# Kernel optimization log

Measured on AMD Instinct MI355X. Metric: run time of the kernel, lower is better.

The kernel has to match this reference:

```python
import jax, jax.numpy as jnp
import numpy as np

N_NODES = 100000

def gcn_conv(x, edge_index, W, b, n_nodes):
    # GCNConv: add self-loops, symmetric normalization D^-1/2 A D^-1/2, then linear.
    loops = jnp.arange(n_nodes, dtype=edge_index.dtype)
    row = jnp.concatenate([edge_index[0], loops])  # source nodes
    col = jnp.concatenate([edge_index[1], loops])  # destination nodes
    deg = jax.ops.segment_sum(jnp.ones_like(col, dtype=x.dtype), col, num_segments=n_nodes)
    dinv = jnp.where(deg > 0, jax.lax.rsqrt(deg), 0.0)
    norm = dinv[row] * dinv[col]                   # [E']
    h = x @ W                                      # [N, out] project first (out dim small)
    msgs = h[row] * norm[:, None]                  # gather + scale
    out = jax.ops.segment_sum(msgs, col, num_segments=n_nodes)  # scatter-add
    return out + b

def setup_inputs() -> dict:
    key = jax.random.key(0)
    k1, k2, k3, k4, k5, k6 = jax.random.split(key, 6)
    in_dim, hid, out_dim = 512, 16, 16
    x = jax.random.normal(k1, (N_NODES, in_dim), dtype=jnp.float32)
    edge_index = jax.random.randint(k2, (2, 3200000), 0, N_NODES, dtype=jnp.int64)
    # Glorot-style init for weights, zero bias (GCNConv defaults)
    W1 = jax.random.normal(k3, (in_dim, hid), dtype=jnp.float32) * (1.0 / np.sqrt(in_dim))
    b1 = jnp.zeros((hid,), dtype=jnp.float32)
    W2 = jax.random.normal(k4, (hid, out_dim), dtype=jnp.float32) * (1.0 / np.sqrt(hid))
    b2 = jnp.zeros((out_dim,), dtype=jnp.float32)
    return {"x": x, "edge_index": edge_index, "W1": W1, "b1": b1, "W2": W2, "b2": b2}

def reference(x, edge_index, W1, b1, W2, b2):
    h = jax.nn.relu(gcn_conv(x, edge_index, W1, b1, N_NODES))
    # dropout is identity in eval mode
    logits = gcn_conv(h, edge_index, W2, b2, N_NODES)
    return jax.nn.log_softmax(logits, axis=1)
```

## Files before the change

kernel.cpp:

```cpp
#include <hip/hip_runtime.h>
#include <cstddef>

typedef unsigned int uint32;
typedef short bf16x8 __attribute__((ext_vector_type(8)));
typedef float f32x4 __attribute__((ext_vector_type(4)));

#define BCAP 5120
#define NBLK 256

__device__ __forceinline__ unsigned short f2bf(float f) {
  unsigned u = __float_as_uint(f);
  unsigned r = (u + 0x7FFFu + ((u >> 16) & 1u)) >> 16;
  return (unsigned short)r;
}
__device__ __forceinline__ float bf_lo(uint32 u) { return __uint_as_float(u << 16); }
__device__ __forceinline__ float bf_hi(uint32 u) { return __uint_as_float(u & 0xFFFF0000u); }

__global__ __launch_bounds__(256) void k_init(
    int* __restrict__ bcur, int NB, const float* __restrict__ W1,
    unsigned short* __restrict__ wfrag) {
  int zb = (NB + 255) >> 8;
  int b = blockIdx.x;
  if (b < zb) {
    int i = b * 256 + threadIdx.x;
    if (i < NB) bcur[i] = i * BCAP;
  } else {
    int i = (b - zb) * 256 + threadIdx.x;
    if (i < 8192) {
      int j = i & 7, o = (i >> 3) & 15, g = (i >> 7) & 3, kt = i >> 9;
      wfrag[i] = f2bf(W1[(kt * 32 + g * 8 + j) * 16 + o]);
    }
  }
}

__global__ __launch_bounds__(1024) void k_bfill(
    const int* __restrict__ row, const int* __restrict__ col,
    int* __restrict__ bcur, int* __restrict__ bedges, int E, int NB, int chunk) {
  __shared__ int s[1024];
  for (int j = threadIdx.x; j < NB; j += 1024) s[j] = 0;
  __syncthreads();
  int lo = blockIdx.x * chunk;
  int hi = lo + chunk; if (hi > E) hi = E;
  for (int k = lo + threadIdx.x; k < hi; k += 1024) atomicAdd(&s[col[k] >> 7], 1);
  __syncthreads();
  for (int j = threadIdx.x; j < NB; j += 1024) {
    int h = s[j];
    s[j] = h ? atomicAdd(&bcur[j], h) : 0;
  }
  __syncthreads();
  for (int k = lo + threadIdx.x; k < hi; k += 1024) {
    int c = col[k];
    int b = c >> 7;
    int slot = atomicAdd(&s[b], 1);
    if (slot < (b + 1) * BCAP)
      bedges[slot] = ((c & 127) << 17) | row[k];
  }
}

__global__ __launch_bounds__(128) void k_bdeg(
    const int* __restrict__ bcur, const int* __restrict__ bedges,
    float* __restrict__ dinv, int n) {
  __shared__ int c[128];
  int b = blockIdx.x, t = threadIdx.x;
  c[t] = 0;
  __syncthreads();
  int k0 = b * BCAP;
  int k1 = bcur[b]; if (k1 > k0 + BCAP) k1 = k0 + BCAP;
  for (int k = k0 + t; k < k1; k += 128)
    atomicAdd(&c[((unsigned)bedges[k]) >> 17], 1);
  __syncthreads();
  int node = b * 128 + t;
  if (node < n) dinv[node] = rsqrtf(1.0f + (float)c[t]);
}

#define GCAP 2048
#define CAPL 48
template <int MODE>
__global__ __launch_bounds__(256) void k_gagg(
    const int* __restrict__ bcur, const int* __restrict__ bedges,
    const uint4* __restrict__ mb,
    float* __restrict__ agg, unsigned short* __restrict__ msgs_out,
    const float* __restrict__ dinv, const float* __restrict__ b1,
    const float* __restrict__ W2, const float* __restrict__ b2, int n) {
  __shared__ int lsrt[CAPL * 128];
  __shared__ int curs[128];
  __shared__ int ovf[128];
  __shared__ int novf;
  __shared__ float w2s[256];
  __shared__ float b1s[16];
  int b = blockIdx.x, t = threadIdx.x;
  if (MODE == 1) {
    w2s[t] = W2[t];
    if (t < 16) b1s[t] = b1[t];
  }
  int j = t >> 1, h = t & 1;
  int node = b * 128 + j;
  float a0 = 0.f, a1 = 0.f, a2 = 0.f, a3 = 0.f;
  float a4 = 0.f, a5 = 0.f, a6 = 0.f, a7 = 0.f;
  if (node < n) {
    float4 sA = *(const float4*)(agg + (size_t)node * 16 + h * 8);
    float4 sB = *(const float4*)(agg + (size_t)node * 16 + h * 8 + 4);
    a0 = sA.x; a1 = sA.y; a2 = sA.z; a3 = sA.w;
    a4 = sB.x; a5 = sB.y; a6 = sB.z; a7 = sB.w;
  }
  int k0 = b * BCAP;
  int k1 = bcur[b]; if (k1 > k0 + BCAP) k1 = k0 + BCAP;
  const uint4* mbh = mb + h;
  for (int base = k0; base < k1; base += GCAP) {
    int cnt = k1 - base; if (cnt > GCAP) cnt = GCAP;
    if (t < 128) curs[t] = 0;
    if (t == 0) novf = 0;
    __syncthreads();
    for (int idx = t; idx < cnt; idx += 256) {
      unsigned e = (unsigned)bedges[base + idx];
      int lc = e >> 17;
      int slot = atomicAdd(&curs[lc], 1);
      if (slot < CAPL) lsrt[slot * 128 + lc] = (int)(e & 0x1FFFF);
      else {
        int oi = atomicAdd(&novf, 1);
        if (oi < 128) ovf[oi] = (int)e;
      }
    }
    __syncthreads();
    int len = curs[j]; if (len > CAPL) len = CAPL;
    int k = 0;
    for (; k + 4 <= len; k += 4) {
      int r0 = lsrt[(k + 0) * 128 + j], r1 = lsrt[(k + 1) * 128 + j];
      int r2 = lsrt[(k + 2) * 128 + j], r3 = lsrt[(k + 3) * 128 + j];
      uint4 v0 = mbh[(size_t)r0 * 2];
      uint4 v1 = mbh[(size_t)r1 * 2];
      uint4 v2 = mbh[(size_t)r2 * 2];
      uint4 v3 = mbh[(size_t)r3 * 2];
      a0 += (bf_lo(v0.x) + bf_lo(v1.x)) + (bf_lo(v2.x) + bf_lo(v3.x));
      a1 += (bf_hi(v0.x) + bf_hi(v1.x)) + (bf_hi(v2.x) + bf_hi(v3.x));
      a2 += (bf_lo(v0.y) + bf_lo(v1.y)) + (bf_lo(v2.y) + bf_lo(v3.y));
      a3 += (bf_hi(v0.y) + bf_hi(v1.y)) + (bf_hi(v2.y) + bf_hi(v3.y));
      a4 += (bf_lo(v0.z) + bf_lo(v1.z)) + (bf_lo(v2.z) + bf_lo(v3.z));
      a5 += (bf_hi(v0.z) + bf_hi(v1.z)) + (bf_hi(v2.z) + bf_hi(v3.z));
      a6 += (bf_lo(v0.w) + bf_lo(v1.w)) + (bf_lo(v2.w) + bf_lo(v3.w));
      a7 += (bf_hi(v0.w) + bf_hi(v1.w)) + (bf_hi(v2.w) + bf_hi(v3.w));
    }
    for (; k < len; ++k) {
      uint4 v = mbh[(size_t)lsrt[k * 128 + j] * 2];
      a0 += bf_lo(v.x); a1 += bf_hi(v.x);
      a2 += bf_lo(v.y); a3 += bf_hi(v.y);
      a4 += bf_lo(v.z); a5 += bf_hi(v.z);
      a6 += bf_lo(v.w); a7 += bf_hi(v.w);
    }
    int no = novf; if (no > 128) no = 128;
    for (int i = 0; i < no; ++i) {
      unsigned e = (unsigned)ovf[i];
      if ((int)(e >> 17) == j) {
        uint4 v = mbh[(size_t)(e & 0x1FFFF) * 2];
        a0 += bf_lo(v.x); a1 += bf_hi(v.x);
        a2 += bf_lo(v.y); a3 += bf_hi(v.y);
        a4 += bf_lo(v.z); a5 += bf_hi(v.z);
        a6 += bf_lo(v.w); a7 += bf_hi(v.w);
      }
    }
    __syncthreads();
  }
  if (node < n) {
    float tot[8] = {a0, a1, a2, a3, a4, a5, a6, a7};
    float di = dinv[node];
    if (MODE == 1) {
      float hh[8];
#pragma unroll
      for (int f = 0; f < 8; ++f)
        hh[f] = fmaxf(fmaf(di, tot[f], b1s[h * 8 + f]), 0.0f);
      float gp[16];
#pragma unroll
      for (int o = 0; o < 16; ++o) gp[o] = 0.0f;
#pragma unroll
      for (int f = 0; f < 8; ++f) {
        float hf = hh[f];
        const float* wrow = &w2s[(h * 8 + f) * 16];
#pragma unroll
        for (int o = 0; o < 16; ++o) gp[o] = fmaf(hf, wrow[o], gp[o]);
      }
      float gv[8];
#pragma unroll
      for (int f = 0; f < 8; ++f) {
        float keep = h ? gp[8 + f] : gp[f];
        float send = h ? gp[f] : gp[8 + f];
        gv[f] = (keep + __shfl_xor(send, 1, 64)) * di;
      }
      uint32 u0 = (uint32)f2bf(gv[0]) | ((uint32)f2bf(gv[1]) << 16);
      uint32 u1 = (uint32)f2bf(gv[2]) | ((uint32)f2bf(gv[3]) << 16);
      uint32 u2 = (uint32)f2bf(gv[4]) | ((uint32)f2bf(gv[5]) << 16);
      uint32 u3 = (uint32)f2bf(gv[6]) | ((uint32)f2bf(gv[7]) << 16);
      uint4 pk; pk.x = u0; pk.y = u1; pk.z = u2; pk.w = u3;
      ((uint4*)msgs_out)[(size_t)node * 2 + h] = pk;
      float4* aw = (float4*)(agg + (size_t)node * 16 + h * 8);
      aw[0] = make_float4(gv[0], gv[1], gv[2], gv[3]);
      aw[1] = make_float4(gv[4], gv[5], gv[6], gv[7]);
    } else {
      float v[8];
#pragma unroll
      for (int f = 0; f < 8; ++f) v[f] = fmaf(di, tot[f], b2[h * 8 + f]);
      float m8 = v[0];
#pragma unroll
      for (int f = 1; f < 8; ++f) m8 = fmaxf(m8, v[f]);
      float m = fmaxf(m8, __shfl_xor(m8, 1, 64));
      float s8 = 0.0f;
#pragma unroll
      for (int f = 0; f < 8; ++f) s8 += expf(v[f] - m);
      float s = s8 + __shfl_xor(s8, 1, 64);
      float ls = logf(s) + m;
      float4* aw = (float4*)(agg + (size_t)node * 16 + h * 8);
      aw[0] = make_float4(v[0] - ls, v[1] - ls, v[2] - ls, v[3] - ls);
      aw[1] = make_float4(v[4] - ls, v[5] - ls, v[6] - ls, v[7] - ls);
    }
  }
}

__global__ __launch_bounds__(256) void k_gemm1_mfma(
    const float* __restrict__ x, const uint4* __restrict__ wf4,
    const float* __restrict__ dinv, unsigned short* __restrict__ msgsb,
    float* __restrict__ agg, int n) {
  int wave = threadIdx.x >> 6, lane = threadIdx.x & 63;
  int m = lane & 15, g = lane >> 4;
  int r0 = (blockIdx.x * 4 + wave) * 16;
  if (r0 >= n) return;

  union BU { uint4 u; bf16x8 v; };
  BU bfr[16];
#pragma unroll
  for (int kt = 0; kt < 16; ++kt) bfr[kt].u = wf4[kt * 64 + g * 16 + m];

  int row = r0 + m;
  int lrow = (row < n) ? row : (n - 1);
  const float* xr = x + (size_t)lrow * 512 + g * 8;

  f32x4 acc = {0.f, 0.f, 0.f, 0.f};
#pragma unroll
  for (int kt = 0; kt < 16; ++kt) {
    float4 xa = *(const float4*)(xr + kt * 32);
    float4 xb = *(const float4*)(xr + kt * 32 + 4);
    union { uint32 u[4]; bf16x8 v; } a;
    a.u[0] = (uint32)f2bf(xa.x) | ((uint32)f2bf(xa.y) << 16);
    a.u[1] = (uint32)f2bf(xa.z) | ((uint32)f2bf(xa.w) << 16);
    a.u[2] = (uint32)f2bf(xb.x) | ((uint32)f2bf(xb.y) << 16);
    a.u[3] = (uint32)f2bf(xb.z) | ((uint32)f2bf(xb.w) << 16);
    acc = __builtin_amdgcn_mfma_f32_16x16x32_bf16(a.v, bfr[kt].v, acc, 0, 0, 0);
  }

#pragma unroll
  for (int j = 0; j < 4; ++j) {
    int orow = r0 + g * 4 + j;
    if (orow < n) {
      float v = acc[j] * dinv[orow];
      agg[(size_t)orow * 16 + m] = v;
      msgsb[(size_t)orow * 16 + m] = f2bf(v);
    }
  }
}


__global__ void k_deg_init(float* __restrict__ deg, int n) {
  int i = blockIdx.x * 256 + threadIdx.x;
  if (i < n) deg[i] = 1.0f;
}

__global__ void k_deg_count(const int* __restrict__ col, float* __restrict__ deg, int E) {
  int e = blockIdx.x * 256 + threadIdx.x;
  if (e < E) atomicAdd(&deg[col[e]], 1.0f);
}

__global__ void k_rsqrt_inplace(float* __restrict__ deg, int n) {
  int i = blockIdx.x * 256 + threadIdx.x;
  if (i < n) deg[i] = rsqrtf(deg[i]);
}

__global__ void k_scatter(const int* __restrict__ row, const int* __restrict__ col,
                          const float* __restrict__ src, float* __restrict__ agg, int E) {
  int t = blockIdx.x * 256 + threadIdx.x;
  int e = t >> 2, q = t & 3;
  if (e >= E) return;
  int r = row[e];
  int c = col[e];
  float4 v = ((const float4*)(src + (size_t)r * 16))[q];
  float* dst = agg + (size_t)c * 16 + q * 4;
  atomicAdd(dst + 0, v.x);
  atomicAdd(dst + 1, v.y);
  atomicAdd(dst + 2, v.z);
  atomicAdd(dst + 3, v.w);
}

__global__ void k_transposeW1(const float* __restrict__ W1, float* __restrict__ wt) {
  int i = blockIdx.x * 256 + threadIdx.x;
  if (i < 512 * 16) {
    int e = i >> 4, f = i & 15;
    wt[f * 512 + e] = W1[i];
  }
}

__global__ __launch_bounds__(256) void k_gemm1(
    const float* __restrict__ x, const float* __restrict__ wt_g,
    const float* __restrict__ dinv,
    float* __restrict__ msgsf, float* __restrict__ agg, int n) {
  __shared__ float4 wt4[16 * 128];
  const float4* wg4 = (const float4*)wt_g;
  for (int k = threadIdx.x; k < 2048; k += 256) wt4[k] = wg4[k];
  __syncthreads();

  int wave = threadIdx.x >> 6, lane = threadIdx.x & 63;
  int r0 = blockIdx.x * 8 + wave * 2;
  if (r0 >= n) return;
  int r1 = (r0 + 1 < n) ? (r0 + 1) : r0;

  const float4* x0 = (const float4*)(x + (size_t)r0 * 512);
  const float4* x1 = (const float4*)(x + (size_t)r1 * 512);
  float4 xa0 = x0[lane], xb0 = x0[64 + lane];
  float4 xa1 = x1[lane], xb1 = x1[64 + lane];

  float acc0[16], acc1[16];
#pragma unroll
  for (int f = 0; f < 16; ++f) {
    float4 wa = wt4[f * 128 + lane];
    float4 wb = wt4[f * 128 + 64 + lane];
    acc0[f] = xa0.x * wa.x + xa0.y * wa.y + xa0.z * wa.z + xa0.w * wa.w +
              xb0.x * wb.x + xb0.y * wb.y + xb0.z * wb.z + xb0.w * wb.w;
    acc1[f] = xa1.x * wa.x + xa1.y * wa.y + xa1.z * wa.z + xa1.w * wa.w +
              xb1.x * wb.x + xb1.y * wb.y + xb1.z * wb.z + xb1.w * wb.w;
  }

#pragma unroll
  for (int s = 0; s < 4; ++s) {
    const int mask = 1 << s;
    const int hm = 8 >> s;
    bool up = (lane & mask) != 0;
#pragma unroll
    for (int i = 0; i < hm; ++i) {
      float s0 = up ? acc0[i] : acc0[i + hm];
      float s1 = up ? acc1[i] : acc1[i + hm];
      float g0 = __shfl_xor(s0, mask, 64);
      float g1 = __shfl_xor(s1, mask, 64);
      acc0[i] = (up ? acc0[i + hm] : acc0[i]) + g0;
      acc1[i] = (up ? acc1[i + hm] : acc1[i]) + g1;
    }
  }
  acc0[0] += __shfl_xor(acc0[0], 16, 64);
  acc0[0] += __shfl_xor(acc0[0], 32, 64);
  acc1[0] += __shfl_xor(acc1[0], 16, 64);
  acc1[0] += __shfl_xor(acc1[0], 32, 64);

  int grp = lane >> 4;
  if (grp < 2) {
    int row = r0 + grp;
    if (row < n) {
      int l4 = lane & 15;
      int f = ((l4 & 1) << 3) | ((l4 & 2) << 1) | ((l4 & 4) >> 1) | ((l4 & 8) >> 3);
      float v = (grp == 0 ? acc0[0] : acc1[0]) * dinv[row];
      msgsf[(size_t)row * 16 + f] = v;
      agg[(size_t)row * 16 + f] = v;
    }
  }
}

__global__ __launch_bounds__(256) void k_mid(
    float* __restrict__ agg, const float* __restrict__ dinv,
    const float* __restrict__ b1, const float* __restrict__ W2,
    float* __restrict__ gpf, int n) {
  __shared__ float w2s[256];
  __shared__ float b1s[16];
  if (threadIdx.x < 256) w2s[threadIdx.x] = W2[threadIdx.x];
  if (threadIdx.x < 16) b1s[threadIdx.x] = b1[threadIdx.x];
  __syncthreads();
  int i = blockIdx.x * 256 + threadIdx.x;
  if (i >= n) return;
  float di = dinv[i];
  float h[16];
  const float4* a4 = (const float4*)(agg + (size_t)i * 16);
#pragma unroll
  for (int q = 0; q < 4; ++q) {
    float4 v = a4[q];
    h[q * 4 + 0] = v.x; h[q * 4 + 1] = v.y; h[q * 4 + 2] = v.z; h[q * 4 + 3] = v.w;
  }
#pragma unroll
  for (int f = 0; f < 16; ++f) h[f] = fmaxf(fmaf(di, h[f], b1s[f]), 0.0f);
  float g[16];
#pragma unroll
  for (int o = 0; o < 16; ++o) g[o] = 0.0f;
#pragma unroll
  for (int f = 0; f < 16; ++f) {
    float hf = h[f];
#pragma unroll
    for (int o = 0; o < 16; ++o) g[o] = fmaf(hf, w2s[f * 16 + o], g[o]);
  }
  float4* gA = (float4*)(gpf + (size_t)i * 16);
  float4* gB = (float4*)(agg + (size_t)i * 16);
#pragma unroll
  for (int q = 0; q < 4; ++q) {
    float4 v;
    v.x = g[q * 4 + 0] * di; v.y = g[q * 4 + 1] * di;
    v.z = g[q * 4 + 2] * di; v.w = g[q * 4 + 3] * di;
    gA[q] = v;
    gB[q] = v;
  }
}

__global__ __launch_bounds__(256) void k_final(
    float* __restrict__ agg, const float* __restrict__ dinv,
    const float* __restrict__ b2, int n) {
  int i = blockIdx.x * 256 + threadIdx.x;
  if (i >= n) return;
  float di = dinv[i];
  float v[16];
  const float4* a4 = (const float4*)(agg + (size_t)i * 16);
#pragma unroll
  for (int q = 0; q < 4; ++q) {
    float4 t = a4[q];
    v[q * 4 + 0] = t.x; v[q * 4 + 1] = t.y; v[q * 4 + 2] = t.z; v[q * 4 + 3] = t.w;
  }
#pragma unroll
  for (int f = 0; f < 16; ++f) v[f] = fmaf(di, v[f], b2[f]);
  float m = v[0];
#pragma unroll
  for (int f = 1; f < 16; ++f) m = fmaxf(m, v[f]);
  float s = 0.0f;
#pragma unroll
  for (int f = 0; f < 16; ++f) s += expf(v[f] - m);
  float ls = logf(s) + m;
  float4* o4 = (float4*)(agg + (size_t)i * 16);
#pragma unroll
  for (int q = 0; q < 4; ++q) {
    float4 t;
    t.x = v[q * 4 + 0] - ls; t.y = v[q * 4 + 1] - ls;
    t.z = v[q * 4 + 2] - ls; t.w = v[q * 4 + 3] - ls;
    o4[q] = t;
  }
}

extern "C" void kernel_launch(void* const* d_in, const int* in_sizes, int n_in,
                              void* d_out, int out_size, void* d_ws, size_t ws_size,
                              hipStream_t stream) {
  const float* x = (const float*)d_in[0];
  const int* ei = (const int*)d_in[1];
  const float* W1 = (const float*)d_in[2];
  const float* b1 = (const float*)d_in[3];
  const float* W2 = (const float*)d_in[4];
  const float* b2 = (const float*)d_in[5];
  float* out = (float*)d_out;

  int n = in_sizes[0] / 512;
  int E = in_sizes[1] / 2;
  const int* row = ei;
  const int* col = ei + E;
  int NB = (n + 127) >> 7;

  auto align1k = [](size_t v) { return (v + 1023) & ~(size_t)1023; };
  char* ws = (char*)d_ws;
  size_t o = 0;
  float* dinv  = (float*)(ws + o); o += align1k((size_t)n * 4);
  unsigned short* wfrag = (unsigned short*)(ws + o); o += align1k(8192 * 2);
  int* bcur    = (int*)(ws + o);   o += align1k((size_t)NB * 4);
  int* bedges  = (int*)(ws + o);   o += align1k((size_t)NB * BCAP * 4);
  unsigned short* msgsb1 = (unsigned short*)(ws + o); o += align1k((size_t)n * 16 * 2);
  unsigned short* msgsb2 = (unsigned short*)(ws + o); o += align1k((size_t)n * 16 * 2);
  size_t needed = o;

  float* agg = out;
  int nb_n = (n + 255) / 256;
  int nb_e = (E + 255) / 256;
  int nb_e4 = (E * 4 + 255) / 256;

  if (ws_size >= needed && n <= 131072 && NB <= 1024) {
    int chunk = (E + NBLK - 1) / NBLK;
    int zb = (NB + 255) >> 8;
    k_init<<<zb + 32, 256, 0, stream>>>(bcur, NB, W1, wfrag);
    k_bfill<<<NBLK, 1024, 0, stream>>>(row, col, bcur, bedges, E, NB, chunk);
    k_bdeg<<<NB, 128, 0, stream>>>(bcur, bedges, dinv, n);
    k_gemm1_mfma<<<(n + 63) / 64, 256, 0, stream>>>(
        x, (const uint4*)wfrag, dinv, msgsb1, agg, n);
    k_gagg<1><<<NB, 256, 0, stream>>>(
        bcur, bedges, (const uint4*)msgsb1, agg, msgsb2, dinv, b1, W2, b2, n);
    k_gagg<2><<<NB, 256, 0, stream>>>(
        bcur, bedges, (const uint4*)msgsb2, agg, nullptr, dinv, b1, W2, b2, n);
  } else {
    size_t o2 = 0;
    float* dinv2 = (float*)(ws + o2); o2 += align1k((size_t)n * 4);
    float* wtg2  = (float*)(ws + o2); o2 += 32768;
    float* msgs2 = (float*)(ws + o2);
    k_deg_init<<<nb_n, 256, 0, stream>>>(dinv2, n);
    k_deg_count<<<nb_e, 256, 0, stream>>>(col, dinv2, E);
    k_rsqrt_inplace<<<nb_n, 256, 0, stream>>>(dinv2, n);
    k_transposeW1<<<32, 256, 0, stream>>>(W1, wtg2);
    k_gemm1<<<(n + 7) / 8, 256, 0, stream>>>(x, wtg2, dinv2, msgs2, agg, n);
    k_scatter<<<nb_e4, 256, 0, stream>>>(row, col, msgs2, agg, E);
    k_mid<<<nb_n, 256, 0, stream>>>(agg, dinv2, b1, W2, msgs2, n);
    k_scatter<<<nb_e4, 256, 0, stream>>>(row, col, msgs2, agg, E);
    k_final<<<nb_n, 256, 0, stream>>>(agg, dinv2, b2, n);
  }
}
```

Baseline: 154.6 us.

## Fuse degree, both aggregations into one cooperative kernel with grid syncs

Replaces the degree kernel and two aggregation kernels with one cooperative kernel. It builds each block's local edge lists in shared memory once, computes dinv, and uses grid syncs between the layer-1 and layer-2 aggregation phases. Because the GEMM now runs before dinv exists, the source-side dinv scaling is applied during aggregation through an extra dinv gather per edge. This saves launches and the repeated edge bucketing, but adds grid-wide barriers, per-edge dinv loads and a larger shared-memory list, which may lower occupancy. NB (~782 blocks) must all be co-resident, otherwise the code falls back to the old kernels.

```diff
diff --git a/kernel.cpp b/kernel.cpp
--- a/kernel.cpp
+++ b/kernel.cpp
@@ -1,5 +1,8 @@
 #include <hip/hip_runtime.h>
+#include <hip/hip_cooperative_groups.h>
 #include <cstddef>
+
+namespace cg = cooperative_groups;
 
 typedef unsigned int uint32;
 typedef short bf16x8 __attribute__((ext_vector_type(8)));
@@ -7,6 +10,7 @@
 
 #define BCAP 5120
 #define NBLK 256
+#define CAPL 72
 
 __device__ __forceinline__ unsigned short f2bf(float f) {
   unsigned u = __float_as_uint(f);
@@ -57,72 +61,182 @@
   }
 }
 
-__global__ __launch_bounds__(128) void k_bdeg(
+__global__ __launch_bounds__(256) void k_gemm1_mfma(
+    const float* __restrict__ x, const uint4* __restrict__ wf4,
+    unsigned short* __restrict__ msgsb, float* __restrict__ agg, int n) {
+  int wave = threadIdx.x >> 6, lane = threadIdx.x & 63;
+  int m = lane & 15, g = lane >> 4;
+  int r0 = (blockIdx.x * 4 + wave) * 16;
+  if (r0 >= n) return;
+
+  union BU { uint4 u; bf16x8 v; };
+  BU bfr[16];
+#pragma unroll
+  for (int kt = 0; kt < 16; ++kt) bfr[kt].u = wf4[kt * 64 + g * 16 + m];
+
+  int row = r0 + m;
+  int lrow = (row < n) ? row : (n - 1);
+  const float* xr = x + (size_t)lrow * 512 + g * 8;
+
+  f32x4 acc = {0.f, 0.f, 0.f, 0.f};
+#pragma unroll
+  for (int kt = 0; kt < 16; ++kt) {
+    float4 xa = *(const float4*)(xr + kt * 32);
+    float4 xb = *(const float4*)(xr + kt * 32 + 4);
+    union { uint32 u[4]; bf16x8 v; } a;
+    a.u[0] = (uint32)f2bf(xa.x) | ((uint32)f2bf(xa.y) << 16);
+    a.u[1] = (uint32)f2bf(xa.z) | ((uint32)f2bf(xa.w) << 16);
+    a.u[2] = (uint32)f2bf(xb.x) | ((uint32)f2bf(xb.y) << 16);
+    a.u[3] = (uint32)f2bf(xb.z) | ((uint32)f2bf(xb.w) << 16);
+    acc = __builtin_amdgcn_mfma_f32_16x16x32_bf16(a.v, bfr[kt].v, acc, 0, 0, 0);
+  }
+#pragma unroll
+  for (int j = 0; j < 4; ++j) {
+    int orow = r0 + g * 4 + j;
+    if (orow < n) {
+      agg[(size_t)orow * 16 + m] = acc[j];
+      msgsb[(size_t)orow * 16 + m] = f2bf(acc[j]);
+    }
+  }
+}
+
+__global__ __launch_bounds__(256) void k_coop(
     const int* __restrict__ bcur, const int* __restrict__ bedges,
-    float* __restrict__ dinv, int n) {
-  __shared__ int c[128];
-  int b = blockIdx.x, t = threadIdx.x;
-  c[t] = 0;
-  __syncthreads();
-  int k0 = b * BCAP;
-  int k1 = bcur[b]; if (k1 > k0 + BCAP) k1 = k0 + BCAP;
-  for (int k = k0 + t; k < k1; k += 128)
-    atomicAdd(&c[((unsigned)bedges[k]) >> 17], 1);
-  __syncthreads();
-  int node = b * 128 + t;
-  if (node < n) dinv[node] = rsqrtf(1.0f + (float)c[t]);
-}
-
-#define GCAP 2048
-#define CAPL 48
-template <int MODE>
-__global__ __launch_bounds__(256) void k_gagg(
-    const int* __restrict__ bcur, const int* __restrict__ bedges,
-    const uint4* __restrict__ mb,
-    float* __restrict__ agg, unsigned short* __restrict__ msgs_out,
-    const float* __restrict__ dinv, const float* __restrict__ b1,
-    const float* __restrict__ W2, const float* __restrict__ b2, int n) {
+    const uint4* __restrict__ mb1, unsigned short* __restrict__ msgsb2,
+    float* __restrict__ agg, float* __restrict__ dinv,
+    const float* __restrict__ b1, const float* __restrict__ W2,
+    const float* __restrict__ b2, int n) {
   __shared__ int lsrt[CAPL * 128];
   __shared__ int curs[128];
   __shared__ int ovf[128];
   __shared__ int novf;
   __shared__ float w2s[256];
   __shared__ float b1s[16];
+  cg::grid_group grid = cg::this_grid();
   int b = blockIdx.x, t = threadIdx.x;
-  if (MODE == 1) {
-    w2s[t] = W2[t];
-    if (t < 16) b1s[t] = b1[t];
-  }
+  w2s[t] = W2[t];
+  if (t < 16) b1s[t] = b1[t];
+  if (t < 128) curs[t] = 0;
+  if (t == 0) novf = 0;
+  __syncthreads();
+
+  int k0 = b * BCAP;
+  int cnt = bcur[b] - k0; if (cnt > BCAP) cnt = BCAP; if (cnt < 0) cnt = 0;
+  for (int idx = t; idx < cnt; idx += 256) {
+    unsigned e = (unsigned)bedges[k0 + idx];
+    int lc = e >> 17;
+    int slot = atomicAdd(&curs[lc], 1);
+    if (slot < CAPL) lsrt[slot * 128 + lc] = (int)(e & 0x1FFFF);
+    else {
+      int oi = atomicAdd(&novf, 1);
+      if (oi < 128) ovf[oi] = (int)e;
+    }
+  }
+  __syncthreads();
+  if (t < 128) {
+    int node = b * 128 + t;
+    if (node < n) dinv[node] = rsqrtf(1.0f + (float)curs[t]);
+  }
+  grid.sync();
+
   int j = t >> 1, h = t & 1;
   int node = b * 128 + j;
-  float a0 = 0.f, a1 = 0.f, a2 = 0.f, a3 = 0.f;
-  float a4 = 0.f, a5 = 0.f, a6 = 0.f, a7 = 0.f;
+  float di = (node < n) ? dinv[node] : 0.0f;
+  int len = 0;
+  if (node < n) { len = curs[j]; if (len > CAPL) len = CAPL; }
+  int no = novf; if (no > 128) no = 128;
+
+  {
+    float a0 = 0.f, a1 = 0.f, a2 = 0.f, a3 = 0.f;
+    float a4 = 0.f, a5 = 0.f, a6 = 0.f, a7 = 0.f;
+    if (node < n) {
+      float4 sA = *(const float4*)(agg + (size_t)node * 16 + h * 8);
+      float4 sB = *(const float4*)(agg + (size_t)node * 16 + h * 8 + 4);
+      a0 = di * sA.x; a1 = di * sA.y; a2 = di * sA.z; a3 = di * sA.w;
+      a4 = di * sB.x; a5 = di * sB.y; a6 = di * sB.z; a7 = di * sB.w;
+      const uint4* mbh = mb1 + h;
+      int k = 0;
+      for (; k + 4 <= len; k += 4) {
+        int r0 = lsrt[(k + 0) * 128 + j], r1 = lsrt[(k + 1) * 128 + j];
+        int r2 = lsrt[(k + 2) * 128 + j], r3 = lsrt[(k + 3) * 128 + j];
+        uint4 v0 = mbh[(size_t)r0 * 2];
+        uint4 v1 = mbh[(size_t)r1 * 2];
+        uint4 v2 = mbh[(size_t)r2 * 2];
+        uint4 v3 = mbh[(size_t)r3 * 2];
+        float d0 = dinv[r0], d1 = dinv[r1], d2 = dinv[r2], d3 = dinv[r3];
+        a0 += (d0 * bf_lo(v0.x) + d1 * bf_lo(v1.x)) + (d2 * bf_lo(v2.x) + d3 * bf_lo(v3.x));
+        a1 += (d0 * bf_hi(v0.x) + d1 * bf_hi(v1.x)) + (d2 * bf_hi(v2.x) + d3 * bf_hi(v3.x));
+        a2 += (d0 * bf_lo(v0.y) + d1 * bf_lo(v1.y)) + (d2 * bf_lo(v2.y) + d3 * bf_lo(v3.y));
+        a3 += (d0 * bf_hi(v0.y) + d1 * bf_hi(v1.y)) + (d2 * bf_hi(v2.y) + d3 * bf_hi(v3.y));
+        a4 += (d0 * bf_lo(v0.z) + d1 * bf_lo(v1.z)) + (d2 * bf_lo(v2.z) + d3 * bf_lo(v3.z));
+        a5 += (d0 * bf_hi(v0.z) + d1 * bf_hi(v1.z)) + (d2 * bf_hi(v2.z) + d3 * bf_hi(v3.z));
+        a6 += (d0 * bf_lo(v0.w) + d1 * bf_lo(v1.w)) + (d2 * bf_lo(v2.w) + d3 * bf_lo(v3.w));
+        a7 += (d0 * bf_hi(v0.w) + d1 * bf_hi(v1.w)) + (d2 * bf_hi(v2.w) + d3 * bf_hi(v3.w));
+      }
+      for (; k < len; ++k) {
+        int r = lsrt[k * 128 + j];
+        uint4 v = mbh[(size_t)r * 2];
+        float d = dinv[r];
+        a0 += d * bf_lo(v.x); a1 += d * bf_hi(v.x);
+        a2 += d * bf_lo(v.y); a3 += d * bf_hi(v.y);
+        a4 += d * bf_lo(v.z); a5 += d * bf_hi(v.z);
+        a6 += d * bf_lo(v.w); a7 += d * bf_hi(v.w);
+      }
+      for (int i = 0; i < no; ++i) {
+        unsigned e = (unsigned)ovf[i];
+        if ((int)(e >> 17) == j) {
+          int r = (int)(e & 0x1FFFF);
+          uint4 v = mbh[(size_t)r * 2];
+          float d = dinv[r];
+          a0 += d * bf_lo(v.x); a1 += d * bf_hi(v.x);
+          a2 += d * bf_lo(v.y); a3 += d * bf_hi(v.y);
+          a4 += d * bf_lo(v.z); a5 += d * bf_hi(v.z);
+          a6 += d * bf_lo(v.w); a7 += d * bf_hi(v.w);
+        }
+      }
+      float tot[8] = {a0, a1, a2, a3, a4, a5, a6, a7};
+      float hh[8];
+#pragma unroll
+      for (int f = 0; f < 8; ++f)
+        hh[f] = fmaxf(fmaf(di, tot[f], b1s[h * 8 + f]), 0.0f);
+      float gp[16];
+#pragma unroll
+      for (int o = 0; o < 16; ++o) gp[o] = 0.0f;
+#pragma unroll
+      for (int f = 0; f < 8; ++f) {
+        float hf = hh[f];
+        const float* wrow = &w2s[(h * 8 + f) * 16];
+#pragma unroll
+        for (int o = 0; o < 16; ++o) gp[o] = fmaf(hf, wrow[o], gp[o]);
+      }
+      float gv[8];
+#pragma unroll
+      for (int f = 0; f < 8; ++f) {
+        float keep = h ? gp[8 + f] : gp[f];
+        float send = h ? gp[f] : gp[8 + f];
+        gv[f] = (keep + __shfl_xor(send, 1, 64)) * di;
+      }
+      uint32 u0 = (uint32)f2bf(gv[0]) | ((uint32)f2bf(gv[1]) << 16);
+      uint32 u1 = (uint32)f2bf(gv[2]) | ((uint32)f2bf(gv[3]) << 16);
+      uint32 u2 = (uint32)f2bf(gv[4]) | ((uint32)f2bf(gv[5]) << 16);
+      uint32 u3 = (uint32)f2bf(gv[6]) | ((uint32)f2bf(gv[7]) << 16);
+      uint4 pk; pk.x = u0; pk.y = u1; pk.z = u2; pk.w = u3;
+      ((uint4*)msgsb2)[(size_t)node * 2 + h] = pk;
+      float4* aw = (float4*)(agg + (size_t)node * 16 + h * 8);
+      aw[0] = make_float4(gv[0], gv[1], gv[2], gv[3]);
+      aw[1] = make_float4(gv[4], gv[5], gv[6], gv[7]);
+    }
+  }
+  __threadfence();
+  grid.sync();
+
   if (node < n) {
+    float a0, a1, a2, a3, a4, a5, a6, a7;
     float4 sA = *(const float4*)(agg + (size_t)node * 16 + h * 8);
     float4 sB = *(const float4*)(agg + (size_t)node * 16 + h * 8 + 4);
     a0 = sA.x; a1 = sA.y; a2 = sA.z; a3 = sA.w;
     a4 = sB.x; a5 = sB.y; a6 = sB.z; a7 = sB.w;
-  }
-  int k0 = b * BCAP;
-  int k1 = bcur[b]; if (k1 > k0 + BCAP) k1 = k0 + BCAP;
-  const uint4* mbh = mb + h;
-  for (int base = k0; base < k1; base += GCAP) {
-    int cnt = k1 - base; if (cnt > GCAP) cnt = GCAP;
-    if (t < 128) curs[t] = 0;
-    if (t == 0) novf = 0;
-    __syncthreads();
-    for (int idx = t; idx < cnt; idx += 256) {
-      unsigned e = (unsigned)bedges[base + idx];
-      int lc = e >> 17;
-      int slot = atomicAdd(&curs[lc], 1);
-      if (slot < CAPL) lsrt[slot * 128 + lc] = (int)(e & 0x1FFFF);
-      else {
-        int oi = atomicAdd(&novf, 1);
-        if (oi < 128) ovf[oi] = (int)e;
-      }
-    }
-    __syncthreads();
-    int len = curs[j]; if (len > CAPL) len = CAPL;
+    const uint4* mbh = (const uint4*)msgsb2 + h;
     int k = 0;
     for (; k + 4 <= len; k += 4) {
       int r0 = lsrt[(k + 0) * 128 + j], r1 = lsrt[(k + 1) * 128 + j];
@@ -147,7 +261,6 @@
       a4 += bf_lo(v.z); a5 += bf_hi(v.z);
       a6 += bf_lo(v.w); a7 += bf_hi(v.w);
     }
-    int no = novf; if (no > 128) no = 128;
     for (int i = 0; i < no; ++i) {
       unsigned e = (unsigned)ovf[i];
       if ((int)(e >> 17) == j) {
@@ -158,11 +271,119 @@
         a6 += bf_lo(v.w); a7 += bf_hi(v.w);
       }
     }
+    float v[8] = {a0, a1, a2, a3, a4, a5, a6, a7};
+#pragma unroll
+    for (int f = 0; f < 8; ++f) v[f] = fmaf(di, v[f], b2[h * 8 + f]);
+    float m8 = v[0];
+#pragma unroll
+    for (int f = 1; f < 8; ++f) m8 = fmaxf(m8, v[f]);
+    float m = fmaxf(m8, __shfl_xor(m8, 1, 64));
+    float s8 = 0.0f;
+#pragma unroll
+    for (int f = 0; f < 8; ++f) s8 += expf(v[f] - m);
+    float s = s8 + __shfl_xor(s8, 1, 64);
+    float ls = logf(s) + m;
+    float4* aw = (float4*)(agg + (size_t)node * 16 + h * 8);
+    aw[0] = make_float4(v[0] - ls, v[1] - ls, v[2] - ls, v[3] - ls);
+    aw[1] = make_float4(v[4] - ls, v[5] - ls, v[6] - ls, v[7] - ls);
+  }
+}
+
+
+__global__ __launch_bounds__(128) void k_bdeg(
+    const int* __restrict__ bcur, const int* __restrict__ bedges,
+    float* __restrict__ dinv, int n) {
+  __shared__ int c[128];
+  int b = blockIdx.x, t = threadIdx.x;
+  c[t] = 0;
+  __syncthreads();
+  int k0 = b * BCAP;
+  int k1 = bcur[b]; if (k1 > k0 + BCAP) k1 = k0 + BCAP;
+  for (int k = k0 + t; k < k1; k += 128)
+    atomicAdd(&c[((unsigned)bedges[k]) >> 17], 1);
+  __syncthreads();
+  int node = b * 128 + t;
+  if (node < n) dinv[node] = rsqrtf(1.0f + (float)c[t]);
+}
+
+#define GCAP 2048
+#define CAPLG 48
+template <int MODE>
+__global__ __launch_bounds__(256) void k_gagg(
+    const int* __restrict__ bcur, const int* __restrict__ bedges,
+    const uint4* __restrict__ mb, float* __restrict__ agg,
+    unsigned short* __restrict__ msgs_out, const float* __restrict__ dinv,
+    const float* __restrict__ b1, const float* __restrict__ W2,
+    const float* __restrict__ b2, int n) {
+  __shared__ int lsrt[CAPLG * 128];
+  __shared__ int curs[128];
+  __shared__ int ovf[128];
+  __shared__ int novf;
+  __shared__ float w2s[256];
+  __shared__ float b1s[16];
+  int b = blockIdx.x, t = threadIdx.x;
+  if (MODE == 1) {
+    w2s[t] = W2[t];
+    if (t < 16) b1s[t] = b1[t];
+  }
+  int j = t >> 1, h = t & 1;
+  int node = b * 128 + j;
+  float di = (node < n) ? dinv[node] : 0.0f;
+  float a0 = 0.f, a1 = 0.f, a2 = 0.f, a3 = 0.f;
+  float a4 = 0.f, a5 = 0.f, a6 = 0.f, a7 = 0.f;
+  if (node < n) {
+    float4 sA = *(const float4*)(agg + (size_t)node * 16 + h * 8);
+    float4 sB = *(const float4*)(agg + (size_t)node * 16 + h * 8 + 4);
+    float ss = (MODE == 1) ? di : 1.0f;
+    a0 = ss * sA.x; a1 = ss * sA.y; a2 = ss * sA.z; a3 = ss * sA.w;
+    a4 = ss * sB.x; a5 = ss * sB.y; a6 = ss * sB.z; a7 = ss * sB.w;
+  }
+  int k0 = b * BCAP;
+  int k1 = bcur[b]; if (k1 > k0 + BCAP) k1 = k0 + BCAP;
+  const uint4* mbh = mb + h;
+  for (int base = k0; base < k1; base += GCAP) {
+    int tc = k1 - base; if (tc > GCAP) tc = GCAP;
+    if (t < 128) curs[t] = 0;
+    if (t == 0) novf = 0;
+    __syncthreads();
+    for (int idx = t; idx < tc; idx += 256) {
+      unsigned e = (unsigned)bedges[base + idx];
+      int lc = e >> 17;
+      int slot = atomicAdd(&curs[lc], 1);
+      if (slot < CAPLG) lsrt[slot * 128 + lc] = (int)(e & 0x1FFFF);
+      else {
+        int oi = atomicAdd(&novf, 1);
+        if (oi < 128) ovf[oi] = (int)e;
+      }
+    }
+    __syncthreads();
+    int len = curs[j]; if (len > CAPLG) len = CAPLG;
+    for (int k = 0; k < len; ++k) {
+      int r = lsrt[k * 128 + j];
+      uint4 v = mbh[(size_t)r * 2];
+      float d = (MODE == 1) ? dinv[r] : 1.0f;
+      a0 += d * bf_lo(v.x); a1 += d * bf_hi(v.x);
+      a2 += d * bf_lo(v.y); a3 += d * bf_hi(v.y);
+      a4 += d * bf_lo(v.z); a5 += d * bf_hi(v.z);
+      a6 += d * bf_lo(v.w); a7 += d * bf_hi(v.w);
+    }
+    int no = novf; if (no > 128) no = 128;
+    for (int i = 0; i < no; ++i) {
+      unsigned e = (unsigned)ovf[i];
+      if ((int)(e >> 17) == j) {
+        int r = (int)(e & 0x1FFFF);
+        uint4 v = mbh[(size_t)r * 2];
+        float d = (MODE == 1) ? dinv[r] : 1.0f;
+        a0 += d * bf_lo(v.x); a1 += d * bf_hi(v.x);
+        a2 += d * bf_lo(v.y); a3 += d * bf_hi(v.y);
+        a4 += d * bf_lo(v.z); a5 += d * bf_hi(v.z);
+        a6 += d * bf_lo(v.w); a7 += d * bf_hi(v.w);
+      }
+    }
     __syncthreads();
   }
   if (node < n) {
     float tot[8] = {a0, a1, a2, a3, a4, a5, a6, a7};
-    float di = dinv[node];
     if (MODE == 1) {
       float hh[8];
 #pragma unroll
@@ -210,48 +431,6 @@
       float4* aw = (float4*)(agg + (size_t)node * 16 + h * 8);
       aw[0] = make_float4(v[0] - ls, v[1] - ls, v[2] - ls, v[3] - ls);
       aw[1] = make_float4(v[4] - ls, v[5] - ls, v[6] - ls, v[7] - ls);
-    }
-  }
-}
-
-__global__ __launch_bounds__(256) void k_gemm1_mfma(
-    const float* __restrict__ x, const uint4* __restrict__ wf4,
-    const float* __restrict__ dinv, unsigned short* __restrict__ msgsb,
-    float* __restrict__ agg, int n) {
-  int wave = threadIdx.x >> 6, lane = threadIdx.x & 63;
-  int m = lane & 15, g = lane >> 4;
-  int r0 = (blockIdx.x * 4 + wave) * 16;
-  if (r0 >= n) return;
-
-  union BU { uint4 u; bf16x8 v; };
-  BU bfr[16];
-#pragma unroll
-  for (int kt = 0; kt < 16; ++kt) bfr[kt].u = wf4[kt * 64 + g * 16 + m];
-
-  int row = r0 + m;
-  int lrow = (row < n) ? row : (n - 1);
-  const float* xr = x + (size_t)lrow * 512 + g * 8;
-
-  f32x4 acc = {0.f, 0.f, 0.f, 0.f};
-#pragma unroll
-  for (int kt = 0; kt < 16; ++kt) {
-    float4 xa = *(const float4*)(xr + kt * 32);
-    float4 xb = *(const float4*)(xr + kt * 32 + 4);
-    union { uint32 u[4]; bf16x8 v; } a;
-    a.u[0] = (uint32)f2bf(xa.x) | ((uint32)f2bf(xa.y) << 16);
-    a.u[1] = (uint32)f2bf(xa.z) | ((uint32)f2bf(xa.w) << 16);
-    a.u[2] = (uint32)f2bf(xb.x) | ((uint32)f2bf(xb.y) << 16);
-    a.u[3] = (uint32)f2bf(xb.z) | ((uint32)f2bf(xb.w) << 16);
-    acc = __builtin_amdgcn_mfma_f32_16x16x32_bf16(a.v, bfr[kt].v, acc, 0, 0, 0);
-  }
-
-#pragma unroll
-  for (int j = 0; j < 4; ++j) {
-    int orow = r0 + g * 4 + j;
-    if (orow < n) {
-      float v = acc[j] * dinv[orow];
-      agg[(size_t)orow * 16 + m] = v;
-      msgsb[(size_t)orow * 16 + m] = f2bf(v);
     }
   }
 }
@@ -470,13 +649,21 @@
     int zb = (NB + 255) >> 8;
     k_init<<<zb + 32, 256, 0, stream>>>(bcur, NB, W1, wfrag);
     k_bfill<<<NBLK, 1024, 0, stream>>>(row, col, bcur, bedges, E, NB, chunk);
-    k_bdeg<<<NB, 128, 0, stream>>>(bcur, bedges, dinv, n);
     k_gemm1_mfma<<<(n + 63) / 64, 256, 0, stream>>>(
-        x, (const uint4*)wfrag, dinv, msgsb1, agg, n);
-    k_gagg<1><<<NB, 256, 0, stream>>>(
-        bcur, bedges, (const uint4*)msgsb1, agg, msgsb2, dinv, b1, W2, b2, n);
-    k_gagg<2><<<NB, 256, 0, stream>>>(
-        bcur, bedges, (const uint4*)msgsb2, agg, nullptr, dinv, b1, W2, b2, n);
+        x, (const uint4*)wfrag, msgsb1, agg, n);
+    const uint4* mb1c = (const uint4*)msgsb1;
+    void* args[] = {(void*)&bcur, (void*)&bedges, (void*)&mb1c, (void*)&msgsb2,
+                    (void*)&agg, (void*)&dinv, (void*)&b1, (void*)&W2,
+                    (void*)&b2, (void*)&n};
+    hipError_t ce = hipLaunchCooperativeKernel(
+        reinterpret_cast<void*>(k_coop), dim3(NB), dim3(256), args, 0, stream);
+    if (ce != hipSuccess) {
+      k_bdeg<<<NB, 128, 0, stream>>>(bcur, bedges, dinv, n);
+      k_gagg<1><<<NB, 256, 0, stream>>>(
+          bcur, bedges, (const uint4*)msgsb1, agg, msgsb2, dinv, b1, W2, b2, n);
+      k_gagg<2><<<NB, 256, 0, stream>>>(
+          bcur, bedges, (const uint4*)msgsb2, agg, nullptr, dinv, b1, W2, b2, n);
+    }
   } else {
     size_t o2 = 0;
     float* dinv2 = (float*)(ws + o2); o2 += align1k((size_t)n * 4);
```

Measured after the change: 399.1 us. 158% more time.
